# Performance work log

Measured on AMD Instinct MI355X. Metric: run time of the kernel, lower is better.

## Reference

```python
import jax, jax.numpy as jnp
import numpy as np

NUM_HEADS = 12


def setup_inputs() -> dict:
    key = jax.random.key(0)
    ks = jax.random.split(key, 6)
    dim = 384
    B, N = 2048, 49
    nW = 64
    return {
        "x": jax.random.normal(ks[0], (B, N, dim), dtype=jnp.float32),
        "mask": jax.random.normal(ks[1], (nW, N, N), dtype=jnp.float32),
        "qkv_w": jax.random.normal(ks[2], (3 * dim, dim), dtype=jnp.float32) * 0.02,
        "qkv_b": jax.random.normal(ks[3], (3 * dim,), dtype=jnp.float32) * 0.02,
        "proj_w": jax.random.normal(ks[4], (dim, dim), dtype=jnp.float32) * 0.02,
        "proj_b": jax.random.normal(ks[5], (dim,), dtype=jnp.float32) * 0.02,
    }


def reference(x, mask, qkv_w, qkv_b, proj_w, proj_b):
    B, N, C = x.shape
    H = NUM_HEADS
    Dh = C // H
    scale = Dh ** -0.5
    nW = mask.shape[0]

    # qkv projection: [B, N, 3C]
    qkv = x @ qkv_w.T + qkv_b
    q, k, v = jnp.split(qkv, 3, axis=-1)

    def heads(t):  # [B, N, C] -> [B, H, N, Dh]
        return t.reshape(B, N, H, Dh).transpose(0, 2, 1, 3)

    q, k, v = heads(q) * scale, heads(k), heads(v)

    # [B, H, N, N] attention scores
    attn = jnp.einsum("bhnd,bhmd->bhnm", q, k)
    # add per-window additive mask: reshape B -> (B//nW, nW)
    attn = attn.reshape(B // nW, nW, H, N, N) + mask[None, :, None, :, :]
    attn = jax.nn.softmax(attn.reshape(B, H, N, N), axis=-1)

    out = jnp.einsum("bhnm,bhmd->bhnd", attn, v)
    out = out.transpose(0, 2, 1, 3).reshape(B, N, C)
    return out @ proj_w.T + proj_b
```

## Files before the change

### kernel.cpp

```cpp
#include <hip/hip_runtime.h>
#include <hip/hip_bf16.h>
#include <stdint.h>

typedef unsigned short u16;
typedef __attribute__((ext_vector_type(8))) short short8;
typedef __attribute__((ext_vector_type(4))) short s4v;
typedef __attribute__((ext_vector_type(4))) float f32x4;

__device__ inline u16 f2bf(float f) {
    union { float f; unsigned int u; } x; x.f = f;
    unsigned int u = x.u;
    unsigned int r = (u + 0x7FFFu + ((u >> 16) & 1u)) >> 16;
    return (u16)r;
}

__device__ inline void gld_lds16(const u16* g, u16* l) {
    auto const* gp = reinterpret_cast<const __attribute__((address_space(1))) unsigned int*>(
        reinterpret_cast<uintptr_t>(g));
    auto* lp = reinterpret_cast<__attribute__((address_space(3))) unsigned int*>(
        reinterpret_cast<uintptr_t>(l));
    __builtin_amdgcn_global_load_lds(gp, lp, 16, 0, 0);
}

#if __has_builtin(__builtin_amdgcn_mfma_f32_16x16x16bf16_1k)
#define MFMA16(a, b, c) __builtin_amdgcn_mfma_f32_16x16x16bf16_1k((a), (b), (c), 0, 0, 0)
#elif __has_builtin(__builtin_amdgcn_mfma_f32_16x16x16_bf16)
#define MFMA16(a, b, c) __builtin_amdgcn_mfma_f32_16x16x16_bf16((a), (b), (c), 0, 0, 0)
#else
__device__ inline f32x4 mfma16_asm(s4v a, s4v b, f32x4 c) {
    asm volatile("s_nop 1\n\tv_mfma_f32_16x16x16_bf16 %0, %1, %2, %0\n\ts_nop 7\n\ts_nop 7"
                 : "+v"(c) : "v"(a), "v"(b));
    return c;
}
#define MFMA16(a, b, c) mfma16_asm((a), (b), (c))
#endif

#define NX8 4816896
#define NQ8 55296
#define NP8 18432
__global__ __launch_bounds__(256) void prep_all(const float* __restrict__ x,
                                                const float* __restrict__ qw,
                                                const float* __restrict__ pw,
                                                u16* __restrict__ xb,
                                                u16* __restrict__ wqr,
                                                u16* __restrict__ wp) {
    size_t i = (size_t)blockIdx.x * 256 + threadIdx.x;
    const float* src; u16* dst; size_t soff, doff;
    if (i < NX8) {
        src = x; dst = xb; soff = i; doff = i;
    } else if (i < NX8 + NQ8) {
        size_t off = i - NX8;
        int orow = (int)(off / 48);
        int chunk = (int)(off - (size_t)orow * 48);
        int sec = orow / 384;
        int rem = orow - sec * 384;
        int hh = rem >> 5, d = rem & 31;
        int nrow = hh * 96 + sec * 32 + d;
        src = qw; dst = wqr; soff = off; doff = (size_t)nrow * 48 + chunk;
    } else {
        src = pw; dst = wp; soff = i - (NX8 + NQ8); doff = soff;
    }
    float4 v0 = ((const float4*)src)[soff * 2];
    float4 v1 = ((const float4*)src)[soff * 2 + 1];
    u16 h[8];
    h[0] = f2bf(v0.x); h[1] = f2bf(v0.y); h[2] = f2bf(v0.z); h[3] = f2bf(v0.w);
    h[4] = f2bf(v1.x); h[5] = f2bf(v1.y); h[6] = f2bf(v1.z); h[7] = f2bf(v1.w);
    *(uint4*)(dst + doff * 8) = *(const uint4*)h;
}

__global__ __launch_bounds__(256, 3) void qkv_attn(const u16* __restrict__ xb,
                                                   const u16* __restrict__ wqr,
                                                   const float* __restrict__ bias,
                                                   const float* __restrict__ mask,
                                                   u16* __restrict__ aout) {
    __shared__ __align__(16) u16 lds[14336];
    u16* Abuf[2] = { lds, lds + 4096 };
    u16* Bbuf[2] = { lds + 8192, lds + 11264 };
    u16* QK = lds;
    u16* Vt = lds + 8704;

    const int tid = threadIdx.x;
    const int wave = tid >> 6, lane = tid & 63;
    const int lr = lane >> 4, lc = lane & 15;
    const int lin = blockIdx.x;
    const int xcd = lin & 7;
    const int idx = lin >> 3;
    const int h = idx % 12;
    const int mp = xcd * 128 + idx / 12;
    const int row0 = mp * 98;

    f32x4 acc[2][6] = {};

    const int srow = lane >> 2, scol = (lane & 3) * 8;
    const int ar0 = row0 + wave * 32 + srow;
    const int ar1 = (ar0 < 100351) ? ar0 : 100351;
    const int ar2 = (ar0 + 16 < 100351) ? ar0 + 16 : 100351;
    const u16* aSrc1 = xb + (size_t)ar1 * 384 + scol;
    const u16* aSrc2 = xb + (size_t)ar2 * 384 + scol;
    const u16* bSrc = wqr + (size_t)(h * 96 + wave * 16 + srow) * 384 + scol;

    auto stage = [&](int k0, int buf) {
        gld_lds16(aSrc1 + k0, Abuf[buf] + wave * 1024);
        gld_lds16(aSrc2 + k0, Abuf[buf] + wave * 1024 + 512);
        gld_lds16(bSrc + k0, Bbuf[buf] + wave * 512);
        if (wave < 2)
            gld_lds16(bSrc + (size_t)64 * 384 + k0, Bbuf[buf] + 2048 + wave * 512);
    };
    auto compute = [&](int buf) {
        short8 af[2], bfr[6];
#pragma unroll
        for (int i = 0; i < 2; ++i)
            af[i] = *(const short8*)&Abuf[buf][(wave * 32 + i * 16 + lc) * 32 + lr * 8];
#pragma unroll
        for (int j = 0; j < 6; ++j)
            bfr[j] = *(const short8*)&Bbuf[buf][(j * 16 + lc) * 32 + lr * 8];
#pragma unroll
        for (int i = 0; i < 2; ++i)
#pragma unroll
            for (int j = 0; j < 6; ++j)
                acc[i][j] = __builtin_amdgcn_mfma_f32_16x16x32_bf16(bfr[j], af[i], acc[i][j], 0, 0, 0);
    };

    stage(0, 0);
    __syncthreads();
#pragma unroll
    for (int t = 0; t < 12; ++t) {
        if (t < 11) stage((t + 1) * 32, (t + 1) & 1);
        compute(t & 1);
        __syncthreads();
    }

    const float scale = 0.17677669529663687f;
#pragma unroll
    for (int j = 0; j < 6; ++j) {
        const int sec = j >> 1;
        const int nb = (j & 1) * 16 + lr * 4;
        float4 bv = *(const float4*)&bias[sec * 384 + h * 32 + nb];
        const float mult = (sec == 0) ? scale : 1.0f;
#pragma unroll
        for (int i = 0; i < 2; ++i) {
            const int m = wave * 32 + i * 16 + lc;
            float v0 = (acc[i][j][0] + bv.x) * mult;
            float v1 = (acc[i][j][1] + bv.y) * mult;
            float v2 = (acc[i][j][2] + bv.z) * mult;
            float v3 = (acc[i][j][3] + bv.w) * mult;
            if (sec < 2) {
                union { u16 h[4]; uint2 u; } pk;
                pk.h[0] = f2bf(v0); pk.h[1] = f2bf(v1);
                pk.h[2] = f2bf(v2); pk.h[3] = f2bf(v3);
                *(uint2*)&QK[m * 68 + sec * 32 + nb] = pk.u;
            } else {
                Vt[(nb + 0) * 132 + m] = f2bf(v0);
                Vt[(nb + 1) * 132 + m] = f2bf(v1);
                Vt[(nb + 2) * 132 + m] = f2bf(v2);
                Vt[(nb + 3) * 132 + m] = f2bf(v3);
            }
        }
    }
    __syncthreads();

    const int winSel = wave & 1, qh = wave >> 1;
    const int woff = winSel * 49;
    const float* mrow = mask + (size_t)((2 * mp + winSel) & 63) * 2401;

    short8 kf[4], qf[2];
    s4v vfA[2][4];
#pragma unroll
    for (int j = 0; j < 4; ++j)
        kf[j] = *(const short8*)&QK[(woff + j * 16 + lc) * 68 + 32 + lr * 8];
#pragma unroll
    for (int ii = 0; ii < 2; ++ii)
        qf[ii] = *(const short8*)&QK[(woff + (qh * 2 + ii) * 16 + lc) * 68 + lr * 8];
#pragma unroll
    for (int nt = 0; nt < 2; ++nt)
#pragma unroll
        for (int sj = 0; sj < 4; ++sj)
            vfA[nt][sj] = *(const s4v*)&Vt[(nt * 16 + lc) * 132 + woff + sj * 16 + lr * 4];

    f32x4 S2[2][4] = {};
#pragma unroll
    for (int ii = 0; ii < 2; ++ii)
#pragma unroll
        for (int sj = 0; sj < 4; ++sj)
            S2[ii][sj] = __builtin_amdgcn_mfma_f32_16x16x32_bf16(kf[sj], qf[ii], S2[ii][sj], 0, 0, 0);

    const size_t orow = (size_t)(row0 + woff) * 384 + h * 32 + lr * 4;
#pragma unroll
    for (int ii = 0; ii < 2; ++ii) {
        const int q = (qh * 2 + ii) * 16 + lc;
        const int im = (q < 49) ? q : 48;
        const float* mq = mrow + im * 49;
        float s = 0.0f;
        s4v pfq[4];
#pragma unroll
        for (int sj = 0; sj < 4; ++sj) {
            const int kbase = sj * 16 + lr * 4;
            s4v pk;
#pragma unroll
            for (int r = 0; r < 4; ++r) {
                const int k = kbase + r;
                float t = (k < 49) ? (S2[ii][sj][r] + mq[k]) : -1e30f;
                float p = __expf(t);
                s += p;
                pk[r] = (short)f2bf(p);
            }
            pfq[sj] = pk;
        }
        s += __shfl_xor(s, 16);
        s += __shfl_xor(s, 32);

        f32x4 O0 = {}, O1 = {};
#pragma unroll
        for (int sj = 0; sj < 4; ++sj) {
            O0 = MFMA16(vfA[0][sj], pfq[sj], O0);
            O1 = MFMA16(vfA[1][sj], pfq[sj], O1);
        }

        if (q < 49) {
            float rl = __builtin_amdgcn_rcpf(s);
            union { u16 h[4]; uint2 u; } pk;
            pk.h[0] = f2bf(O0[0] * rl); pk.h[1] = f2bf(O0[1] * rl);
            pk.h[2] = f2bf(O0[2] * rl); pk.h[3] = f2bf(O0[3] * rl);
            *(uint2*)(aout + orow + (size_t)q * 384) = pk.u;
            pk.h[0] = f2bf(O1[0] * rl); pk.h[1] = f2bf(O1[1] * rl);
            pk.h[2] = f2bf(O1[2] * rl); pk.h[3] = f2bf(O1[3] * rl);
            *(uint2*)(aout + orow + (size_t)q * 384 + 16) = pk.u;
        }
    }
}

__global__ __launch_bounds__(256) void proj_gemm(const u16* __restrict__ a,
                                                 const u16* __restrict__ wp,
                                                 const float* __restrict__ bias,
                                                 float* __restrict__ out) {
    __shared__ u16 As[2][128 * 32];
    __shared__ u16 Bs[2][128 * 32];
    const int tid = threadIdx.x;
    const int wave = tid >> 6, lane = tid & 63;
    const int lr = lane >> 4, lc = lane & 15;
    const int wm = (wave & 1) * 64, wn = (wave >> 1) * 64;
    const int lin = blockIdx.x;
    const int xcd = lin & 7;
    const int idx = lin >> 3;
    const int nBase = (idx % 3) * 128;
    const int mBase = (xcd * 98 + idx / 3) * 128;

    f32x4 acc[4][4] = {};

    const int srow = lane >> 2, scol = (lane & 3) * 8;
    const u16* aSrc = a  + (size_t)(mBase + wave * 32 + srow) * 384 + scol;
    const u16* bSrc = wp + (size_t)(nBase + wave * 32 + srow) * 384 + scol;

    auto stage = [&](int k0, int buf) {
        u16* aDst = &As[buf][wave * 1024];
        u16* bDst = &Bs[buf][wave * 1024];
        gld_lds16(aSrc + k0, aDst);
        gld_lds16(aSrc + k0 + (size_t)16 * 384, aDst + 512);
        gld_lds16(bSrc + k0, bDst);
        gld_lds16(bSrc + k0 + (size_t)16 * 384, bDst + 512);
    };
    auto compute = [&](int buf) {
        short8 af[4], bfr[4];
#pragma unroll
        for (int i = 0; i < 4; ++i)
            af[i] = *(const short8*)&As[buf][(wm + i * 16 + lc) * 32 + lr * 8];
#pragma unroll
        for (int j = 0; j < 4; ++j)
            bfr[j] = *(const short8*)&Bs[buf][(wn + j * 16 + lc) * 32 + lr * 8];
#pragma unroll
        for (int i = 0; i < 4; ++i)
#pragma unroll
            for (int j = 0; j < 4; ++j)
                acc[i][j] = __builtin_amdgcn_mfma_f32_16x16x32_bf16(bfr[j], af[i], acc[i][j], 0, 0, 0);
    };

    stage(0, 0);
    __syncthreads();
#pragma unroll
    for (int t = 0; t < 11; ++t) {
        stage((t + 1) * 32, (t + 1) & 1);
        compute(t & 1);
        __syncthreads();
    }
    compute(11 & 1);

#pragma unroll
    for (int j = 0; j < 4; ++j) {
        int gnb = nBase + wn + j * 16 + lr * 4;
        float4 bv = *(const float4*)&bias[gnb];
#pragma unroll
        for (int i = 0; i < 4; ++i) {
            int gm = mBase + wm + i * 16 + lc;
            float4 o;
            o.x = acc[i][j][0] + bv.x;
            o.y = acc[i][j][1] + bv.y;
            o.z = acc[i][j][2] + bv.z;
            o.w = acc[i][j][3] + bv.w;
            *(float4*)(out + (size_t)gm * 384 + gnb) = o;
        }
    }
}

extern "C" void kernel_launch(void* const* d_in, const int* in_sizes, int n_in,
                              void* d_out, int out_size, void* d_ws, size_t ws_size,
                              hipStream_t stream) {
    const float* x      = (const float*)d_in[0];
    const float* mask   = (const float*)d_in[1];
    const float* qkv_w  = (const float*)d_in[2];
    const float* qkv_b  = (const float*)d_in[3];
    const float* proj_w = (const float*)d_in[4];
    const float* proj_b = (const float*)d_in[5];
    float* out = (float*)d_out;

    char* ws = (char*)d_ws;
    u16* wqr  = (u16*)ws;
    u16* wp   = (u16*)(ws + 884736);
    u16* attn = (u16*)(ws + 1179648);
    u16* xb   = (u16*)(ws + 232390656);

    prep_all<<<19104, 256, 0, stream>>>(x, qkv_w, proj_w, xb, wqr, wp);
    qkv_attn<<<12288, 256, 0, stream>>>(xb, wqr, qkv_b, mask, attn);
    proj_gemm<<<2352, 256, 0, stream>>>(attn, wp, proj_b, out);
}
```

Measured before the change: 509.2 us.

## Process two heads per block in fused QKV-attention kernel to reuse x tiles

Each block now computes QKV projections for two heads instead of one, halving the grid and letting each staged x tile feed twice as many MFMAs. Attention is then split so each wave handles one window for one head across all query rows. The aim is to cut redundant global loads of the activation matrix. In exchange, the accumulator array doubles to 96 floats per lane and LDS grows to about 50KB, which may lower occupancy below the launch-bounds target of 3 blocks.

```diff
diff --git a/kernel.cpp b/kernel.cpp
--- a/kernel.cpp
+++ b/kernel.cpp
@@ -73,11 +73,11 @@
                                                    const float* __restrict__ bias,
                                                    const float* __restrict__ mask,
                                                    u16* __restrict__ aout) {
-    __shared__ __align__(16) u16 lds[14336];
+    __shared__ __align__(16) u16 lds[25216];
     u16* Abuf[2] = { lds, lds + 4096 };
-    u16* Bbuf[2] = { lds + 8192, lds + 11264 };
+    u16* Bbuf[2] = { lds + 8192, lds + 14336 };
     u16* QK = lds;
-    u16* Vt = lds + 8704;
+    u16* Vt = lds + 16896;
 
     const int tid = threadIdx.x;
     const int wave = tid >> 6, lane = tid & 63;
@@ -85,11 +85,11 @@
     const int lin = blockIdx.x;
     const int xcd = lin & 7;
     const int idx = lin >> 3;
-    const int h = idx % 12;
-    const int mp = xcd * 128 + idx / 12;
+    const int hp = idx % 6;
+    const int mp = xcd * 128 + idx / 6;
     const int row0 = mp * 98;
 
-    f32x4 acc[2][6] = {};
+    f32x4 acc[2][12] = {};
 
     const int srow = lane >> 2, scol = (lane & 3) * 8;
     const int ar0 = row0 + wave * 32 + srow;
@@ -97,28 +97,33 @@
     const int ar2 = (ar0 + 16 < 100351) ? ar0 + 16 : 100351;
     const u16* aSrc1 = xb + (size_t)ar1 * 384 + scol;
     const u16* aSrc2 = xb + (size_t)ar2 * 384 + scol;
-    const u16* bSrc = wqr + (size_t)(h * 96 + wave * 16 + srow) * 384 + scol;
+    const u16* bSrc = wqr + (size_t)(hp * 192 + wave * 48 + srow) * 384 + scol;
 
     auto stage = [&](int k0, int buf) {
         gld_lds16(aSrc1 + k0, Abuf[buf] + wave * 1024);
         gld_lds16(aSrc2 + k0, Abuf[buf] + wave * 1024 + 512);
-        gld_lds16(bSrc + k0, Bbuf[buf] + wave * 512);
-        if (wave < 2)
-            gld_lds16(bSrc + (size_t)64 * 384 + k0, Bbuf[buf] + 2048 + wave * 512);
+        gld_lds16(bSrc + k0,                    Bbuf[buf] + wave * 1536);
+        gld_lds16(bSrc + (size_t)16 * 384 + k0, Bbuf[buf] + wave * 1536 + 512);
+        gld_lds16(bSrc + (size_t)32 * 384 + k0, Bbuf[buf] + wave * 1536 + 1024);
     };
     auto compute = [&](int buf) {
-        short8 af[2], bfr[6];
+        short8 af[2];
 #pragma unroll
         for (int i = 0; i < 2; ++i)
             af[i] = *(const short8*)&Abuf[buf][(wave * 32 + i * 16 + lc) * 32 + lr * 8];
 #pragma unroll
-        for (int j = 0; j < 6; ++j)
-            bfr[j] = *(const short8*)&Bbuf[buf][(j * 16 + lc) * 32 + lr * 8];
-#pragma unroll
-        for (int i = 0; i < 2; ++i)
-#pragma unroll
-            for (int j = 0; j < 6; ++j)
-                acc[i][j] = __builtin_amdgcn_mfma_f32_16x16x32_bf16(bfr[j], af[i], acc[i][j], 0, 0, 0);
+        for (int half = 0; half < 2; ++half) {
+            short8 bfr[6];
+#pragma unroll
+            for (int j6 = 0; j6 < 6; ++j6)
+                bfr[j6] = *(const short8*)&Bbuf[buf][((half * 6 + j6) * 16 + lc) * 32 + lr * 8];
+#pragma unroll
+            for (int i = 0; i < 2; ++i)
+#pragma unroll
+                for (int j6 = 0; j6 < 6; ++j6)
+                    acc[i][half * 6 + j6] =
+                        __builtin_amdgcn_mfma_f32_16x16x32_bf16(bfr[j6], af[i], acc[i][half * 6 + j6], 0, 0, 0);
+        }
     };
 
     stage(0, 0);
@@ -132,10 +137,11 @@
 
     const float scale = 0.17677669529663687f;
 #pragma unroll
-    for (int j = 0; j < 6; ++j) {
-        const int sec = j >> 1;
+    for (int j = 0; j < 12; ++j) {
+        const int hsel = j / 6;
+        const int sec = (j % 6) >> 1;
         const int nb = (j & 1) * 16 + lr * 4;
-        float4 bv = *(const float4*)&bias[sec * 384 + h * 32 + nb];
+        float4 bv = *(const float4*)&bias[sec * 384 + (2 * hp + hsel) * 32 + nb];
         const float mult = (sec == 0) ? scale : 1.0f;
 #pragma unroll
         for (int i = 0; i < 2; ++i) {
@@ -148,46 +154,49 @@
                 union { u16 h[4]; uint2 u; } pk;
                 pk.h[0] = f2bf(v0); pk.h[1] = f2bf(v1);
                 pk.h[2] = f2bf(v2); pk.h[3] = f2bf(v3);
-                *(uint2*)&QK[m * 68 + sec * 32 + nb] = pk.u;
+                *(uint2*)&QK[hsel * 8448 + m * 66 + sec * 32 + nb] = pk.u;
             } else {
-                Vt[(nb + 0) * 132 + m] = f2bf(v0);
-                Vt[(nb + 1) * 132 + m] = f2bf(v1);
-                Vt[(nb + 2) * 132 + m] = f2bf(v2);
-                Vt[(nb + 3) * 132 + m] = f2bf(v3);
+                u16* vt = Vt + hsel * 4160;
+                vt[(nb + 0) * 130 + m] = f2bf(v0);
+                vt[(nb + 1) * 130 + m] = f2bf(v1);
+                vt[(nb + 2) * 130 + m] = f2bf(v2);
+                vt[(nb + 3) * 130 + m] = f2bf(v3);
             }
         }
     }
     __syncthreads();
 
-    const int winSel = wave & 1, qh = wave >> 1;
+    const int winSel = wave & 1, hsel = wave >> 1;
     const int woff = winSel * 49;
+    const int h = 2 * hp + hsel;
     const float* mrow = mask + (size_t)((2 * mp + winSel) & 63) * 2401;
-
-    short8 kf[4], qf[2];
+    const u16* QKh = QK + hsel * 8448;
+    const u16* Vth = Vt + hsel * 4160;
+
+    short8 qf[4], kf[4];
     s4v vfA[2][4];
 #pragma unroll
-    for (int j = 0; j < 4; ++j)
-        kf[j] = *(const short8*)&QK[(woff + j * 16 + lc) * 68 + 32 + lr * 8];
-#pragma unroll
-    for (int ii = 0; ii < 2; ++ii)
-        qf[ii] = *(const short8*)&QK[(woff + (qh * 2 + ii) * 16 + lc) * 68 + lr * 8];
+    for (int i = 0; i < 4; ++i) {
+        qf[i] = *(const short8*)&QKh[(woff + i * 16 + lc) * 66 + lr * 8];
+        kf[i] = *(const short8*)&QKh[(woff + i * 16 + lc) * 66 + 32 + lr * 8];
+    }
 #pragma unroll
     for (int nt = 0; nt < 2; ++nt)
 #pragma unroll
         for (int sj = 0; sj < 4; ++sj)
-            vfA[nt][sj] = *(const s4v*)&Vt[(nt * 16 + lc) * 132 + woff + sj * 16 + lr * 4];
-
-    f32x4 S2[2][4] = {};
-#pragma unroll
-    for (int ii = 0; ii < 2; ++ii)
+            vfA[nt][sj] = *(const s4v*)&Vth[(nt * 16 + lc) * 130 + woff + sj * 16 + lr * 4];
+
+    f32x4 S2[4][4] = {};
+#pragma unroll
+    for (int si = 0; si < 4; ++si)
 #pragma unroll
         for (int sj = 0; sj < 4; ++sj)
-            S2[ii][sj] = __builtin_amdgcn_mfma_f32_16x16x32_bf16(kf[sj], qf[ii], S2[ii][sj], 0, 0, 0);
+            S2[si][sj] = __builtin_amdgcn_mfma_f32_16x16x32_bf16(kf[sj], qf[si], S2[si][sj], 0, 0, 0);
 
     const size_t orow = (size_t)(row0 + woff) * 384 + h * 32 + lr * 4;
 #pragma unroll
-    for (int ii = 0; ii < 2; ++ii) {
-        const int q = (qh * 2 + ii) * 16 + lc;
+    for (int si = 0; si < 4; ++si) {
+        const int q = si * 16 + lc;
         const int im = (q < 49) ? q : 48;
         const float* mq = mrow + im * 49;
         float s = 0.0f;
@@ -199,7 +208,7 @@
 #pragma unroll
             for (int r = 0; r < 4; ++r) {
                 const int k = kbase + r;
-                float t = (k < 49) ? (S2[ii][sj][r] + mq[k]) : -1e30f;
+                float t = (k < 49) ? (S2[si][sj][r] + mq[k]) : -1e30f;
                 float p = __expf(t);
                 s += p;
                 pk[r] = (short)f2bf(p);
@@ -319,6 +328,6 @@
     u16* xb   = (u16*)(ws + 232390656);
 
     prep_all<<<19104, 256, 0, stream>>>(x, qkv_w, proj_w, xb, wqr, wp);
-    qkv_attn<<<12288, 256, 0, stream>>>(xb, wqr, qkv_b, mask, attn);
+    qkv_attn<<<6144, 256, 0, stream>>>(xb, wqr, qkv_b, mask, attn);
     proj_gemm<<<2352, 256, 0, stream>>>(attn, wp, proj_b, out);
 }
```

Measured after the change: 524.0 us. +2.9%, slower.
